# Kernel optimization log

Measured on AMD Instinct MI355X. Metric: run time of the kernel, lower is better.

## Reference

```python
import jax, jax.numpy as jnp
import numpy as np

B, S, H, A = 64, 2048, 512, 512


def setup_inputs() -> dict:
    key = jax.random.key(0)
    k1, k2, k3, k4, k5 = jax.random.split(key, 5)
    nn_outs = jax.random.normal(k1, (B, S, H), dtype=jnp.float32)
    # lengths in [1, S] so every row has at least one valid step
    batch_lens = jax.random.randint(k2, (B,), 1, S + 1, dtype=jnp.int64)
    # learned params: context vector ~ U(-0.1, 0.1), Linear(H -> A)
    context = jax.random.uniform(k3, (A,), dtype=jnp.float32, minval=-0.1, maxval=0.1)
    proj_w = jax.random.uniform(k4, (A, H), dtype=jnp.float32, minval=-0.1, maxval=0.1)
    proj_b = jax.random.uniform(k5, (A,), dtype=jnp.float32, minval=-0.1, maxval=0.1)
    return {"nn_outs": nn_outs, "batch_lens": batch_lens,
            "context": context, "proj_w": proj_w, "proj_b": proj_b}


def reference(nn_outs, batch_lens, context, proj_w, proj_b):
    # proj = tanh(Linear(nn_outs)): (B, S, A)
    proj = jnp.tanh(jnp.einsum('bsh,ah->bsa', nn_outs, proj_w) + proj_b)
    # attention scores: (B, S)
    scores = jnp.einsum('bsa,a->bs', proj, context)
    # variable-length masked softmax (replaces the per-batch python loop)
    mask = jnp.arange(nn_outs.shape[1])[None, :] < batch_lens[:, None]  # (B, S)
    scores = jnp.where(mask, scores, -jnp.inf)
    atten = jax.nn.softmax(scores, axis=-1)
    atten = jnp.where(mask, atten, 0.0)  # padded positions exactly zero
    # weighted sum over steps: (B, H)
    return jnp.einsum('bs,bsh->bh', atten, nn_outs)
```

## Files before the change

### kernel.cpp

```cpp
#include <hip/hip_runtime.h>

#define BB 64
#define SS 2048
#define HH 512
#define MROWS (BB*SS)

typedef __attribute__((ext_vector_type(8))) short short8;
typedef __attribute__((ext_vector_type(4))) float f32x4;

__device__ inline unsigned short f2bf(float f){
  unsigned int u = __float_as_uint(f);
  u += 0x7FFFu + ((u >> 16) & 1u);
  return (unsigned short)(u >> 16);
}

__device__ inline int read_len(const void* lens, int i){
  const int* p = (const int*)lens;
  if (p[1] == 0) return (int)((const long long*)lens)[i];
  return p[i];
}

__device__ inline float fast_tanh(float x){
  x = fminf(fmaxf(x, -15.f), 15.f);
  float e = __expf(2.f * x);
  return (e - 1.f) / (e + 1.f);
}

__device__ inline void gload16(const void* gptr, void* lptr){
  __builtin_amdgcn_global_load_lds(
      (const __attribute__((address_space(1))) void*)gptr,
      (__attribute__((address_space(3))) void*)lptr, 16, 0, 0);
}

__device__ inline short8 cvt8p(float4 x0, float4 x1){
  short8 r;
  r[0] = (short)f2bf(x0.x); r[1] = (short)f2bf(x0.y);
  r[2] = (short)f2bf(x0.z); r[3] = (short)f2bf(x0.w);
  r[4] = (short)f2bf(x1.x); r[5] = (short)f2bf(x1.y);
  r[6] = (short)f2bf(x1.z); r[7] = (short)f2bf(x1.w);
  return r;
}

__global__ __launch_bounds__(256) void convw_kernel(
    const float* __restrict__ W, unsigned short* __restrict__ Wb)
{
  size_t base = (size_t)blockIdx.x * 64 * HH;
  int t = threadIdx.x;
  #pragma unroll
  for (int j = 0; j < 32; j++) {
    size_t idx = base + (size_t)j * 1024 + t * 4;
    float4 v = *(const float4*)(W + idx);
    unsigned int p0 = (unsigned int)f2bf(v.x) | ((unsigned int)f2bf(v.y) << 16);
    unsigned int p1 = (unsigned int)f2bf(v.z) | ((unsigned int)f2bf(v.w) << 16);
    *(uint2*)(Wb + idx) = make_uint2(p0, p1);
  }
}

__global__ __launch_bounds__(512, 2) void scores_v11(
    const float* __restrict__ X, const unsigned short* __restrict__ Wb,
    const void* __restrict__ lens, const float* __restrict__ ctx,
    const float* __restrict__ pb, float* __restrict__ scr)
{
  int bid = blockIdx.x;
  int mtile = (bid & 7) * 128 + (bid >> 3);
  int s_start = (mtile * 128) & (SS - 1);
  int b = (mtile * 128) >> 11;
  if (s_start >= read_len(lens, b)) return;

  __shared__ __align__(16) unsigned short As[2][128 * 64];
  __shared__ __align__(16) unsigned short Bs[2][512 * 64];

  int tid = threadIdx.x;
  int lane = tid & 63;
  int w = tid >> 6;
  int wm = w >> 2, wn = w & 3;
  int l15 = lane & 15, g = lane >> 4;

  f32x4 acc[4][8];
  #pragma unroll
  for (int i = 0; i < 4; i++)
    #pragma unroll
    for (int j = 0; j < 8; j++) acc[i][j] = (f32x4)0.f;

  int arow = tid >> 2;
  int alg0 = (tid & 3) * 2;
  const float* Ag = X + (size_t)(mtile * 128 + arow) * HH + alg0 * 8;
  int apg0 = (alg0)     ^ (arow & 7);
  int apg1 = (alg0 + 1) ^ (arow & 7);

  int brow = lane >> 3;
  int blg = (lane & 7) ^ brow;
  const unsigned short* Bg = Wb + (size_t)brow * HH + blg * 8;

  float4 ar[4];

#define A_ISSUE(KT) { const float* p_ = Ag + (KT); \
    ar[0] = *(const float4*)p_;       ar[1] = *(const float4*)(p_ + 4); \
    ar[2] = *(const float4*)(p_ + 8); ar[3] = *(const float4*)(p_ + 12); }

#define A_WRITE(BUF) { \
    *(short8*)&As[BUF][arow * 64 + apg0 * 8] = cvt8p(ar[0], ar[1]); \
    *(short8*)&As[BUF][arow * 64 + apg1 * 8] = cvt8p(ar[2], ar[3]); }

#define B_ISSUE(BUF, KT) { _Pragma("unroll") for (int i_ = 0; i_ < 8; i_++) { \
    int j_ = w * 8 + i_; \
    gload16(Bg + (size_t)(j_ * 8) * HH + (KT), &Bs[BUF][(j_ * 8) * 64]); } }

  A_ISSUE(0)
  B_ISSUE(0, 0)
  A_WRITE(0)
  __syncthreads();

  int cur = 0;
  for (int t = 0; t < 8; ++t) {
    if (t < 7) {
      A_ISSUE((t + 1) * 64)
      B_ISSUE(cur ^ 1, (t + 1) * 64)
    }
    #pragma unroll
    for (int kk = 0; kk < 64; kk += 32) {
      int ga = g + (kk >> 3);
      int pga = (ga ^ (l15 & 7)) * 8;
      short8 af[4];
      #pragma unroll
      for (int im = 0; im < 4; im++) {
        int r = wm * 64 + im * 16 + l15;
        af[im] = *(const short8*)&As[cur][r * 64 + pga];
      }
      #pragma unroll
      for (int in = 0; in < 8; in++) {
        int r2 = wn * 128 + in * 16 + l15;
        short8 bfr = *(const short8*)&Bs[cur][r2 * 64 + pga];
        #pragma unroll
        for (int im = 0; im < 4; im++)
          acc[im][in] = __builtin_amdgcn_mfma_f32_16x16x32_bf16(
              af[im], bfr, acc[im][in], 0, 0, 0);
      }
    }
    if (t < 7) A_WRITE(cur ^ 1)
    __syncthreads();
    cur ^= 1;
  }

  float pbv[8], ctxv[8];
  #pragma unroll
  for (int in = 0; in < 8; in++) {
    int a_g = wn * 128 + in * 16 + l15;
    pbv[in] = pb[a_g];
    ctxv[in] = ctx[a_g];
  }
  float* red = (float*)As;
  #pragma unroll
  for (int im = 0; im < 4; im++) {
    #pragma unroll
    for (int r = 0; r < 4; r++) {
      float rowsum = 0.f;
      #pragma unroll
      for (int in = 0; in < 8; in++)
        rowsum += fast_tanh(acc[im][in][r] + pbv[in]) * ctxv[in];
      #pragma unroll
      for (int m = 1; m < 16; m <<= 1)
        rowsum += __shfl_xor(rowsum, m, 64);
      if (l15 == 0)
        red[wn * 128 + wm * 64 + im * 16 + g * 4 + r] = rowsum;
    }
  }
  __syncthreads();
  if (tid < 128) {
    float s = red[tid] + red[128 + tid] + red[256 + tid] + red[384 + tid];
    scr[(size_t)mtile * 128 + tid] = s;
  }
}

__global__ __launch_bounds__(256) void wsum2_kernel(
    const float* __restrict__ X, const float* __restrict__ scr,
    const void* __restrict__ lens, float* __restrict__ op)
{
  int sc = blockIdx.x;
  int b  = blockIdx.y;
  int tid = threadIdx.x;
  int s0 = sc * 128;
  int len = read_len(lens, b);
  int cnt = min(128, len - s0);
  float* o = op + ((size_t)sc * BB + b) * HH;
  if (cnt <= 0) {
    *(float2*)(o + tid * 2) = make_float2(0.f, 0.f);
    return;
  }

  __shared__ float redm[4], reds[4];
  __shared__ float wsh[128];
  __shared__ f32x4 red[128];

  int wv = tid >> 6, lane = tid & 63;
  float scv[8];
  float m = -1e30f;
  #pragma unroll
  for (int i = 0; i < 8; i++) {
    int s = tid + i * 256;
    scv[i] = scr[(size_t)b * SS + s];
    if (s < len) m = fmaxf(m, scv[i]);
  }
  #pragma unroll
  for (int off = 1; off < 64; off <<= 1) m = fmaxf(m, __shfl_xor(m, off, 64));
  if (lane == 0) redm[wv] = m;
  __syncthreads();
  m = fmaxf(fmaxf(redm[0], redm[1]), fmaxf(redm[2], redm[3]));
  float sum = 0.f;
  #pragma unroll
  for (int i = 0; i < 8; i++) {
    int s = tid + i * 256;
    sum += (s < len) ? __expf(scv[i] - m) : 0.f;
  }
  #pragma unroll
  for (int off = 1; off < 64; off <<= 1) sum += __shfl_xor(sum, off, 64);
  if (lane == 0) reds[wv] = sum;
  __syncthreads();
  float inv = 1.f / (reds[0] + reds[1] + reds[2] + reds[3]);

  if (tid < 128) {
    int s = s0 + tid;
    wsh[tid] = (s < len) ? __expf(scr[(size_t)b * SS + s] - m) * inv : 0.f;
  }
  __syncthreads();

  int h = (tid & 127) * 4;
  int sr = tid >> 7;
  f32x4 acc = (f32x4)0.f;
  for (int i = sr; i < cnt; i += 2) {
    float wvv = wsh[i];
    const float* xr = X + ((size_t)b * SS + s0 + i) * HH + h;
    float4 xv = *(const float4*)xr;
    acc[0] += wvv * xv.x;
    acc[1] += wvv * xv.y;
    acc[2] += wvv * xv.z;
    acc[3] += wvv * xv.w;
  }
  if (sr == 1) red[tid & 127] = acc;
  __syncthreads();
  if (sr == 0) {
    f32x4 r2 = red[tid];
    acc[0] += r2[0]; acc[1] += r2[1]; acc[2] += r2[2]; acc[3] += r2[3];
    *(f32x4*)(o + h) = acc;
  }
}

__global__ __launch_bounds__(512) void reduce_kernel(
    const float* __restrict__ op, float* __restrict__ out)
{
  int b = blockIdx.x;
  int h = threadIdx.x;
  float v = 0.f;
  #pragma unroll
  for (int sc = 0; sc < 16; sc++) v += op[((size_t)sc * BB + b) * HH + h];
  out[(size_t)b * HH + h] = v;
}

__global__ __launch_bounds__(256) void scores_fb(
    const float* __restrict__ X, const void* __restrict__ lens,
    const float* __restrict__ ctx, const float* __restrict__ W,
    const float* __restrict__ pb, float* __restrict__ sp)
{
  int bid = blockIdx.x;
  int wg = (bid & 7) * 512 + (bid >> 3);
  int ntile = wg & 3;
  int mtile = wg >> 2;
  int s_start = (mtile * 128) & (SS - 1);
  int b = (mtile * 128) >> 11;
  if (s_start >= read_len(lens, b)) return;

  __shared__ unsigned short As[128 * 72];
  __shared__ unsigned short Bs[128 * 72];

  int tid = threadIdx.x;
  int lane = tid & 63;
  int w = tid >> 6;
  int wm = w >> 1, wn = w & 1;
  int l15 = lane & 15, g = lane >> 4;

  f32x4 acc[4][4];
  #pragma unroll
  for (int i = 0; i < 4; i++)
    #pragma unroll
    for (int j = 0; j < 4; j++) acc[i][j] = (f32x4)0.f;

  int srow = tid >> 4;
  int scol = (tid & 15) * 4;
  const float* Xbase = X + (size_t)(mtile * 128) * HH;
  const float* Wbase = W + (size_t)(ntile * 128) * HH;

  for (int kt = 0; kt < HH; kt += 64) {
    #pragma unroll
    for (int i = 0; i < 8; i++) {
      int row = srow + i * 16;
      float4 va = *(const float4*)(Xbase + (size_t)row * HH + kt + scol);
      unsigned int p0 = (unsigned int)f2bf(va.x) | ((unsigned int)f2bf(va.y) << 16);
      unsigned int p1 = (unsigned int)f2bf(va.z) | ((unsigned int)f2bf(va.w) << 16);
      *(uint2*)&As[row * 72 + scol] = make_uint2(p0, p1);
      float4 vb = *(const float4*)(Wbase + (size_t)row * HH + kt + scol);
      unsigned int q0 = (unsigned int)f2bf(vb.x) | ((unsigned int)f2bf(vb.y) << 16);
      unsigned int q1 = (unsigned int)f2bf(vb.z) | ((unsigned int)f2bf(vb.w) << 16);
      *(uint2*)&Bs[row * 72 + scol] = make_uint2(q0, q1);
    }
    __syncthreads();
    #pragma unroll
    for (int kk = 0; kk < 64; kk += 32) {
      short8 af[4], bfr[4];
      int ko = kk + g * 8;
      #pragma unroll
      for (int im = 0; im < 4; im++)
        af[im] = *(const short8*)&As[(wm * 64 + im * 16 + l15) * 72 + ko];
      #pragma unroll
      for (int in = 0; in < 4; in++)
        bfr[in] = *(const short8*)&Bs[(wn * 64 + in * 16 + l15) * 72 + ko];
      #pragma unroll
      for (int im = 0; im < 4; im++)
        #pragma unroll
        for (int in = 0; in < 4; in++)
          acc[im][in] = __builtin_amdgcn_mfma_f32_16x16x32_bf16(
              af[im], bfr[in], acc[im][in], 0, 0, 0);
    }
    __syncthreads();
  }

  #pragma unroll
  for (int im = 0; im < 4; im++) {
    #pragma unroll
    for (int r = 0; r < 4; r++) {
      float rowsum = 0.f;
      #pragma unroll
      for (int in = 0; in < 4; in++) {
        int a_g = ntile * 128 + wn * 64 + in * 16 + l15;
        rowsum += fast_tanh(acc[im][in][r] + pb[a_g]) * ctx[a_g];
      }
      #pragma unroll
      for (int m = 1; m < 16; m <<= 1)
        rowsum += __shfl_xor(rowsum, m, 64);
      if (l15 == 0) {
        int rowg = mtile * 128 + wm * 64 + im * 16 + g * 4 + r;
        sp[(size_t)(ntile * 2 + wn) * MROWS + rowg] = rowsum;
      }
    }
  }
}

__global__ __launch_bounds__(256) void softmax8_kernel(
    const float* __restrict__ sp, const void* __restrict__ lens,
    float* __restrict__ wts)
{
  int b = blockIdx.x;
  int tid = threadIdx.x;
  int len = read_len(lens, b);
  float sc[8];
  #pragma unroll
  for (int i = 0; i < 8; i++) {
    int s = tid + i * 256;
    size_t row = (size_t)b * SS + s;
    float v = 0.f;
    #pragma unroll
    for (int p = 0; p < 8; p++) v += sp[(size_t)p * MROWS + row];
    sc[i] = v;
  }
  float m = -1e30f;
  #pragma unroll
  for (int i = 0; i < 8; i++)
    if (tid + i * 256 < len) m = fmaxf(m, sc[i]);
  #pragma unroll
  for (int off = 1; off < 64; off <<= 1) m = fmaxf(m, __shfl_xor(m, off, 64));
  __shared__ float redm[4];
  __shared__ float reds[4];
  int w = tid >> 6, lane = tid & 63;
  if (lane == 0) redm[w] = m;
  __syncthreads();
  m = fmaxf(fmaxf(redm[0], redm[1]), fmaxf(redm[2], redm[3]));
  float e[8]; float sum = 0.f;
  #pragma unroll
  for (int i = 0; i < 8; i++) {
    int s = tid + i * 256;
    e[i] = (s < len) ? __expf(sc[i] - m) : 0.f;
    sum += e[i];
  }
  #pragma unroll
  for (int off = 1; off < 64; off <<= 1) sum += __shfl_xor(sum, off, 64);
  if (lane == 0) reds[w] = sum;
  __syncthreads();
  sum = reds[0] + reds[1] + reds[2] + reds[3];
  float inv = 1.f / sum;
  #pragma unroll
  for (int i = 0; i < 8; i++) {
    int s = tid + i * 256;
    wts[(size_t)b * SS + s] = e[i] * inv;
  }
}

__global__ __launch_bounds__(256) void wsum_fb(
    const float* __restrict__ X, const float* __restrict__ wts,
    const void* __restrict__ lens, float* __restrict__ op)
{
  int sc = blockIdx.x;
  int b  = blockIdx.y;
  int tid = threadIdx.x;
  int s0 = sc * 128;
  int len = read_len(lens, b);
  int cnt = min(128, len - s0);
  float* o = op + ((size_t)sc * BB + b) * HH;
  if (cnt <= 0) {
    *(float2*)(o + tid * 2) = make_float2(0.f, 0.f);
    return;
  }
  __shared__ float wsh[128];
  __shared__ f32x4 red[128];
  if (tid < 128) wsh[tid] = wts[(size_t)b * SS + s0 + tid];
  __syncthreads();
  int h = (tid & 127) * 4;
  int sr = tid >> 7;
  f32x4 acc = (f32x4)0.f;
  for (int i = sr; i < cnt; i += 2) {
    float wv = wsh[i];
    const float* xr = X + ((size_t)b * SS + s0 + i) * HH + h;
    float4 xv = *(const float4*)xr;
    acc[0] += wv * xv.x;
    acc[1] += wv * xv.y;
    acc[2] += wv * xv.z;
    acc[3] += wv * xv.w;
  }
  if (sr == 1) red[tid & 127] = acc;
  __syncthreads();
  if (sr == 0) {
    f32x4 r2 = red[tid];
    acc[0] += r2[0]; acc[1] += r2[1]; acc[2] += r2[2]; acc[3] += r2[3];
    *(f32x4*)(o + h) = acc;
  }
}

extern "C" void kernel_launch(void* const* d_in, const int* in_sizes, int n_in,
                              void* d_out, int out_size, void* d_ws, size_t ws_size,
                              hipStream_t stream) {
  const float* X   = (const float*)d_in[0];
  const void*  lens = d_in[1];
  const float* ctx = (const float*)d_in[2];
  const float* W   = (const float*)d_in[3];
  const float* pb  = (const float*)d_in[4];
  float* out = (float*)d_out;

  char* ws = (char*)d_ws;
  const size_t WB_BYTES = (size_t)HH * HH * 2;
  const size_t SC_BYTES = (size_t)MROWS * 4;
  const size_t OP_BYTES = 16ull * BB * HH * 4;
  const size_t NEED = WB_BYTES + SC_BYTES + OP_BYTES;

  if (ws_size >= NEED) {
    unsigned short* Wb = (unsigned short*)ws;
    float* scr = (float*)(ws + WB_BYTES);
    float* op  = (float*)(ws + WB_BYTES + SC_BYTES);

    convw_kernel<<<8, 256, 0, stream>>>(W, Wb);
    scores_v11<<<1024, 512, 0, stream>>>(X, Wb, lens, ctx, pb, scr);
    wsum2_kernel<<<dim3(16, BB), 256, 0, stream>>>(X, scr, lens, op);
    reduce_kernel<<<BB, 512, 0, stream>>>(op, out);
  } else {
    const size_t SP_BYTES = 8ull * MROWS * 4;
    const size_t WT_BYTES = (size_t)BB * SS * 4;
    float* sp  = (float*)ws;
    float* wts = (float*)(ws + SP_BYTES);
    float* op  = (float*)(ws + SP_BYTES + WT_BYTES);

    scores_fb<<<4096, 256, 0, stream>>>(X, lens, ctx, W, pb, sp);
    softmax8_kernel<<<BB, 256, 0, stream>>>(sp, lens, wts);
    wsum_fb<<<dim3(16, BB), 256, 0, stream>>>(X, wts, lens, op);
    reduce_kernel<<<BB, 512, 0, stream>>>(op, out);
  }
}
```

Measured before the change: 133.2 us.

## Split score GEMM over two N-halves and load X fragments straight to registers

The scores kernel now covers half of the projection outputs per block (2048 blocks, each with a 256-wide N tile), writing two partial score arrays that the weighted-sum kernel adds together. The A operand is no longer staged through shared memory: each wave loads fp32 rows of X directly into registers and converts them to bf16 per MFMA fragment. The B tile is single-buffered with a sync per k-step, and launch bounds rise to 4 blocks per CU. The aim is higher occupancy and less LDS, at the cost of reading X twice, non-coalesced row-wise global loads, and losing the double-buffered prefetch overlap.

```diff
diff --git a/kernel.cpp b/kernel.cpp
--- a/kernel.cpp
+++ b/kernel.cpp
@@ -56,19 +56,19 @@
   }
 }
 
-__global__ __launch_bounds__(512, 2) void scores_v11(
+__global__ __launch_bounds__(512, 4) void scores_v12(
     const float* __restrict__ X, const unsigned short* __restrict__ Wb,
     const void* __restrict__ lens, const float* __restrict__ ctx,
-    const float* __restrict__ pb, float* __restrict__ scr)
+    const float* __restrict__ pb, float* __restrict__ scrp)
 {
   int bid = blockIdx.x;
-  int mtile = (bid & 7) * 128 + (bid >> 3);
+  int ntile = bid & 1;
+  int mtile = bid >> 1;
   int s_start = (mtile * 128) & (SS - 1);
   int b = (mtile * 128) >> 11;
   if (s_start >= read_len(lens, b)) return;
 
-  __shared__ __align__(16) unsigned short As[2][128 * 64];
-  __shared__ __align__(16) unsigned short Bs[2][512 * 64];
+  __shared__ __align__(16) unsigned short Bs[256 * 64];
 
   int tid = threadIdx.x;
   int lane = tid & 63;
@@ -76,87 +76,70 @@
   int wm = w >> 2, wn = w & 3;
   int l15 = lane & 15, g = lane >> 4;
 
-  f32x4 acc[4][8];
+  f32x4 acc[4][4];
   #pragma unroll
   for (int i = 0; i < 4; i++)
     #pragma unroll
-    for (int j = 0; j < 8; j++) acc[i][j] = (f32x4)0.f;
-
-  int arow = tid >> 2;
-  int alg0 = (tid & 3) * 2;
-  const float* Ag = X + (size_t)(mtile * 128 + arow) * HH + alg0 * 8;
-  int apg0 = (alg0)     ^ (arow & 7);
-  int apg1 = (alg0 + 1) ^ (arow & 7);
+    for (int j = 0; j < 4; j++) acc[i][j] = (f32x4)0.f;
+
+  const float* Arow[4];
+  #pragma unroll
+  for (int im = 0; im < 4; im++)
+    Arow[im] = X + (size_t)(mtile * 128 + wm * 64 + im * 16 + l15) * HH + g * 8;
 
   int brow = lane >> 3;
   int blg = (lane & 7) ^ brow;
-  const unsigned short* Bg = Wb + (size_t)brow * HH + blg * 8;
-
-  float4 ar[4];
-
-#define A_ISSUE(KT) { const float* p_ = Ag + (KT); \
-    ar[0] = *(const float4*)p_;       ar[1] = *(const float4*)(p_ + 4); \
-    ar[2] = *(const float4*)(p_ + 8); ar[3] = *(const float4*)(p_ + 12); }
-
-#define A_WRITE(BUF) { \
-    *(short8*)&As[BUF][arow * 64 + apg0 * 8] = cvt8p(ar[0], ar[1]); \
-    *(short8*)&As[BUF][arow * 64 + apg1 * 8] = cvt8p(ar[2], ar[3]); }
-
-#define B_ISSUE(BUF, KT) { _Pragma("unroll") for (int i_ = 0; i_ < 8; i_++) { \
-    int j_ = w * 8 + i_; \
-    gload16(Bg + (size_t)(j_ * 8) * HH + (KT), &Bs[BUF][(j_ * 8) * 64]); } }
-
-  A_ISSUE(0)
-  B_ISSUE(0, 0)
-  A_WRITE(0)
-  __syncthreads();
-
-  int cur = 0;
+  const unsigned short* Bg =
+      Wb + (size_t)(ntile * 256 + w * 32 + brow) * HH + blg * 8;
+
+#define B_ISSUE(KT) { _Pragma("unroll") for (int i_ = 0; i_ < 4; i_++) { \
+    gload16(Bg + (size_t)(i_ * 8) * HH + (KT), &Bs[(w * 32 + i_ * 8) * 64]); } }
+
   for (int t = 0; t < 8; ++t) {
-    if (t < 7) {
-      A_ISSUE((t + 1) * 64)
-      B_ISSUE(cur ^ 1, (t + 1) * 64)
-    }
+    int kt = t * 64;
+    B_ISSUE(kt)
+    __syncthreads();
     #pragma unroll
     for (int kk = 0; kk < 64; kk += 32) {
+      float4 a0[4], a1[4];
+      #pragma unroll
+      for (int im = 0; im < 4; im++) {
+        const float* p = Arow[im] + kt + kk;
+        a0[im] = *(const float4*)p;
+        a1[im] = *(const float4*)(p + 4);
+      }
       int ga = g + (kk >> 3);
-      int pga = (ga ^ (l15 & 7)) * 8;
       short8 af[4];
       #pragma unroll
-      for (int im = 0; im < 4; im++) {
-        int r = wm * 64 + im * 16 + l15;
-        af[im] = *(const short8*)&As[cur][r * 64 + pga];
-      }
-      #pragma unroll
-      for (int in = 0; in < 8; in++) {
-        int r2 = wn * 128 + in * 16 + l15;
-        short8 bfr = *(const short8*)&Bs[cur][r2 * 64 + pga];
+      for (int im = 0; im < 4; im++) af[im] = cvt8p(a0[im], a1[im]);
+      #pragma unroll
+      for (int in = 0; in < 4; in++) {
+        int r2 = wn * 64 + in * 16 + l15;
+        short8 bfr = *(const short8*)&Bs[r2 * 64 + ((ga ^ (r2 & 7))) * 8];
         #pragma unroll
         for (int im = 0; im < 4; im++)
           acc[im][in] = __builtin_amdgcn_mfma_f32_16x16x32_bf16(
               af[im], bfr, acc[im][in], 0, 0, 0);
       }
     }
-    if (t < 7) A_WRITE(cur ^ 1)
     __syncthreads();
-    cur ^= 1;
-  }
-
-  float pbv[8], ctxv[8];
-  #pragma unroll
-  for (int in = 0; in < 8; in++) {
-    int a_g = wn * 128 + in * 16 + l15;
+  }
+
+  float pbv[4], ctxv[4];
+  #pragma unroll
+  for (int in = 0; in < 4; in++) {
+    int a_g = ntile * 256 + wn * 64 + in * 16 + l15;
     pbv[in] = pb[a_g];
     ctxv[in] = ctx[a_g];
   }
-  float* red = (float*)As;
+  float* red = (float*)Bs;
   #pragma unroll
   for (int im = 0; im < 4; im++) {
     #pragma unroll
     for (int r = 0; r < 4; r++) {
       float rowsum = 0.f;
       #pragma unroll
-      for (int in = 0; in < 8; in++)
+      for (int in = 0; in < 4; in++)
         rowsum += fast_tanh(acc[im][in][r] + pbv[in]) * ctxv[in];
       #pragma unroll
       for (int m = 1; m < 16; m <<= 1)
@@ -168,12 +151,12 @@
   __syncthreads();
   if (tid < 128) {
     float s = red[tid] + red[128 + tid] + red[256 + tid] + red[384 + tid];
-    scr[(size_t)mtile * 128 + tid] = s;
+    scrp[(size_t)ntile * MROWS + (size_t)mtile * 128 + tid] = s;
   }
 }
 
 __global__ __launch_bounds__(256) void wsum2_kernel(
-    const float* __restrict__ X, const float* __restrict__ scr,
+    const float* __restrict__ X, const float* __restrict__ scrp,
     const void* __restrict__ lens, float* __restrict__ op)
 {
   int sc = blockIdx.x;
@@ -192,13 +175,17 @@
   __shared__ float wsh[128];
   __shared__ f32x4 red[128];
 
+  const float* sp0 = scrp;
+  const float* sp1 = scrp + MROWS;
+
   int wv = tid >> 6, lane = tid & 63;
   float scv[8];
   float m = -1e30f;
   #pragma unroll
   for (int i = 0; i < 8; i++) {
     int s = tid + i * 256;
-    scv[i] = scr[(size_t)b * SS + s];
+    size_t idx = (size_t)b * SS + s;
+    scv[i] = sp0[idx] + sp1[idx];
     if (s < len) m = fmaxf(m, scv[i]);
   }
   #pragma unroll
@@ -220,7 +207,8 @@
 
   if (tid < 128) {
     int s = s0 + tid;
-    wsh[tid] = (s < len) ? __expf(scr[(size_t)b * SS + s] - m) * inv : 0.f;
+    size_t idx = (size_t)b * SS + s;
+    wsh[tid] = (s < len) ? __expf(sp0[idx] + sp1[idx] - m) * inv : 0.f;
   }
   __syncthreads();
 
@@ -444,19 +432,19 @@
   float* out = (float*)d_out;
 
   char* ws = (char*)d_ws;
-  const size_t WB_BYTES = (size_t)HH * HH * 2;
-  const size_t SC_BYTES = (size_t)MROWS * 4;
-  const size_t OP_BYTES = 16ull * BB * HH * 4;
-  const size_t NEED = WB_BYTES + SC_BYTES + OP_BYTES;
+  const size_t WB_BYTES  = (size_t)HH * HH * 2;
+  const size_t SP2_BYTES = 2ull * MROWS * 4;
+  const size_t OP_BYTES  = 16ull * BB * HH * 4;
+  const size_t NEED = WB_BYTES + SP2_BYTES + OP_BYTES;
 
   if (ws_size >= NEED) {
     unsigned short* Wb = (unsigned short*)ws;
-    float* scr = (float*)(ws + WB_BYTES);
-    float* op  = (float*)(ws + WB_BYTES + SC_BYTES);
+    float* scrp = (float*)(ws + WB_BYTES);
+    float* op   = (float*)(ws + WB_BYTES + SP2_BYTES);
 
     convw_kernel<<<8, 256, 0, stream>>>(W, Wb);
-    scores_v11<<<1024, 512, 0, stream>>>(X, Wb, lens, ctx, pb, scr);
-    wsum2_kernel<<<dim3(16, BB), 256, 0, stream>>>(X, scr, lens, op);
+    scores_v12<<<2048, 512, 0, stream>>>(X, Wb, lens, ctx, pb, scrp);
+    wsum2_kernel<<<dim3(16, BB), 256, 0, stream>>>(X, scrp, lens, op);
     reduce_kernel<<<BB, 512, 0, stream>>>(op, out);
   } else {
     const size_t SP_BYTES = 8ull * MROWS * 4;
```

New measurement: 308.0 us. 131% more time.
